# Kernel optimization log

Measured on AMD Instinct MI355X. Metric: run time of the kernel, lower is better.

## Reference

```python
import jax, jax.numpy as jnp
import numpy as np

D_MODEL = 1024
N_HEADS = 16
D_HEAD = D_MODEL // N_HEADS
QLEN = 512
MLEN = 512
BATCH = 8


def setup_inputs() -> dict:
    key = jax.random.key(0)
    ks = jax.random.split(key, 12)
    s = 0.02
    inputs = jax.random.normal(ks[0], (QLEN, BATCH, D_MODEL), jnp.float32)
    r = jax.random.normal(ks[1], (QLEN + MLEN, 1, D_MODEL), jnp.float32)
    u = jax.random.normal(ks[2], (N_HEADS, D_HEAD), jnp.float32) * s
    v = jax.random.normal(ks[3], (N_HEADS, D_HEAD), jnp.float32) * s
    mem = jax.random.normal(ks[4], (MLEN, BATCH, D_MODEL), jnp.float32)
    # attention params (Transformer-XL style): fused qkv, r-projection, output proj
    W_qkv = jax.random.normal(ks[5], (D_MODEL, 3 * D_MODEL), jnp.float32) * s
    W_r = jax.random.normal(ks[6], (D_MODEL, D_MODEL), jnp.float32) * s
    W_o = jax.random.normal(ks[7], (D_MODEL, D_MODEL), jnp.float32) * s
    # GRU params: input-hidden and hidden-hidden for gates (r, z, n), torch layout
    W_ih = jax.random.normal(ks[8], (3 * D_MODEL, D_MODEL), jnp.float32) * s
    W_hh = jax.random.normal(ks[9], (3 * D_MODEL, D_MODEL), jnp.float32) * s
    b_ih = jax.random.normal(ks[10], (3 * D_MODEL,), jnp.float32) * s
    b_hh = jax.random.normal(ks[11], (3 * D_MODEL,), jnp.float32) * s
    h0 = jnp.zeros((BATCH, D_MODEL), jnp.float32)
    return dict(inputs=inputs, r=r, u=u, v=v, mem=mem, W_qkv=W_qkv, W_r=W_r,
                W_o=W_o, W_ih=W_ih, W_hh=W_hh, b_ih=b_ih, b_hh=b_hh, h0=h0)


def _rel_shift(x):
    # x: [q, k, b, h] -> Transformer-XL relative shift
    q, k, b, h = x.shape
    zero_pad = jnp.zeros((q, 1, b, h), x.dtype)
    x_padded = jnp.concatenate([zero_pad, x], axis=1)        # [q, k+1, b, h]
    x_padded = x_padded.reshape(k + 1, q, b, h)
    return x_padded[1:].reshape(q, k, b, h)


def _attention(inputs, r, u, v, mem, W_qkv, W_r, W_o):
    qlen, bsz, _ = inputs.shape
    cat = jnp.concatenate([mem, inputs], axis=0)             # [klen, b, d]
    klen = cat.shape[0]
    qkv = cat @ W_qkv                                        # [klen, b, 3d]
    w_head_q, w_head_k, w_head_v = jnp.split(qkv, 3, axis=-1)
    w_head_q = w_head_q[-qlen:]                              # [q, b, d]
    r_head_k = (r[:, 0, :] @ W_r).reshape(klen, N_HEADS, D_HEAD)  # [k, h, dh]

    q_ = w_head_q.reshape(qlen, bsz, N_HEADS, D_HEAD)
    k_ = w_head_k.reshape(klen, bsz, N_HEADS, D_HEAD)
    v_ = w_head_v.reshape(klen, bsz, N_HEADS, D_HEAD)

    AC = jnp.einsum('ibhd,jbhd->ijbh', q_ + u[None, None], k_)
    BD = jnp.einsum('ibhd,jhd->ijbh', q_ + v[None, None], r_head_k)
    BD = _rel_shift(BD)
    scale = 1.0 / np.sqrt(D_HEAD)
    attn_score = (AC + BD) * scale                           # [q, k, b, h]

    # causal mask with memory: query i attends to keys j <= i + mlen
    mlen = klen - qlen
    i = jnp.arange(qlen)[:, None]
    j = jnp.arange(klen)[None, :]
    mask = j > (i + mlen)                                    # [q, k]
    attn_score = jnp.where(mask[:, :, None, None], -jnp.inf, attn_score)

    attn_prob = jax.nn.softmax(attn_score, axis=1)
    attn_vec = jnp.einsum('ijbh,jbhd->ibhd', attn_prob, v_)
    attn_vec = attn_vec.reshape(qlen, bsz, D_MODEL)
    return attn_vec @ W_o                                    # [q, b, d]


def _gru(x, h0, W_ih, W_hh, b_ih, b_hh):
    # x: [T, B, D]; torch GRU cell math
    Wi_r, Wi_z, Wi_n = jnp.split(W_ih, 3, axis=0)
    Wh_r, Wh_z, Wh_n = jnp.split(W_hh, 3, axis=0)
    bi_r, bi_z, bi_n = jnp.split(b_ih, 3)
    bh_r, bh_z, bh_n = jnp.split(b_hh, 3)

    # precompute input projections for all timesteps
    xr = x @ Wi_r.T + bi_r
    xz = x @ Wi_z.T + bi_z
    xn = x @ Wi_n.T + bi_n

    def step(h, xs):
        xr_t, xz_t, xn_t = xs
        r = jax.nn.sigmoid(xr_t + h @ Wh_r.T + bh_r)
        z = jax.nn.sigmoid(xz_t + h @ Wh_z.T + bh_z)
        n = jnp.tanh(xn_t + r * (h @ Wh_n.T + bh_n))
        h_new = (1.0 - z) * n + z * h
        return h_new, h_new

    _, ys = jax.lax.scan(step, h0, (xr, xz, xn))
    return ys                                                # [T, B, D]


def reference(inputs, r, u, v, mem, W_qkv, W_r, W_o, W_ih, W_hh, b_ih, b_hh, h0):
    y = _attention(inputs, r, u, v, mem, W_qkv, W_r, W_o)
    return _gru(y, h0, W_ih, W_hh, b_ih, b_hh)
```

## Files before the change

### kernel.cpp

```cpp
#include <hip/hip_runtime.h>
#include <math.h>


typedef short bf16x8 __attribute__((ext_vector_type(8)));
typedef float f32x4 __attribute__((ext_vector_type(4)));

union FragU { uint4 u; bf16x8 h; };

__device__ inline void split2(float x0, float x1, unsigned& hi, unsigned& lo) {
    unsigned u0 = __float_as_uint(x0), u1 = __float_as_uint(x1);
    float h0 = __uint_as_float(u0 & 0xffff0000u);
    float h1 = __uint_as_float(u1 & 0xffff0000u);
    unsigned l0 = __float_as_uint(x0 - h0), l1 = __float_as_uint(x1 - h1);
    hi = (u0 >> 16) | (u1 & 0xffff0000u);
    lo = (l0 >> 16) | (l1 & 0xffff0000u);
}

template<bool TR>
__global__ __launch_bounds__(256) void prep_w(
    const float* __restrict__ W, unsigned* __restrict__ out, int Nr, int K, int ldw)
{
    int idx = blockIdx.x * 256 + threadIdx.x;
    int cpr = K >> 3;
    if (idx >= Nr * cpr) return;
    int n, c;
    if (TR) { n = idx % Nr; c = idx / Nr; }
    else    { c = idx % cpr; n = idx / cpr; }
    int kt = c >> 2, j = c & 3;
    int k = kt * 32 + j * 8;
    float x[8];
    #pragma unroll
    for (int i = 0; i < 8; ++i)
        x[i] = TR ? W[(size_t)(k + i) * ldw + n] : W[(size_t)n * ldw + k + i];
    unsigned h[4], l[4];
    split2(x[0], x[1], h[0], l[0]);
    split2(x[2], x[3], h[1], l[1]);
    split2(x[4], x[5], h[2], l[2]);
    split2(x[6], x[7], h[3], l[3]);
    unsigned* base = out + (size_t)n * K + kt * 32;
    *(uint4*)(base + (((2 * j) ^ (n & 7)) * 4))     = make_uint4(h[0], h[1], h[2], h[3]);
    *(uint4*)(base + (((2 * j + 1) ^ (n & 7)) * 4)) = make_uint4(l[0], l[1], l[2], l[3]);
}

template<int AMODE, bool BIAS>
__global__ __launch_bounds__(256) void gemm_mfma(
    const float* __restrict__ A, const float* __restrict__ A2,
    const unsigned* __restrict__ Bp, const float* __restrict__ bias,
    float* __restrict__ C, int M, int N, int K, int lda, int ldc)
{
    __shared__ uint4 Ab[1024];
    __shared__ uint4 Bb[1024];
    int tid = threadIdx.x;
    int lane = tid & 63, wid = tid >> 6;
    int wr = wid >> 1, wc = wid & 1;
    int n0 = blockIdx.x * 128, m0 = blockIdx.y * 128;
    int r15 = lane & 15, s = lane >> 4;

    f32x4 acc[4][4];
    #pragma unroll
    for (int i = 0; i < 4; ++i)
        #pragma unroll
        for (int j = 0; j < 4; ++j) acc[i][j] = 0.0f;

    for (int kt = 0; kt < (K >> 5); ++kt) {
        int k0 = kt * 32;
        #pragma unroll
        for (int q = 0; q < 2; ++q) {
            int idx = q * 256 + tid;
            int row = idx >> 2, j = idx & 3;
            const float* ap;
            if (AMODE == 1) {
                int gm = m0 + row;
                ap = (gm < 4096) ? (A + (size_t)gm * lda) : (A2 + (size_t)(gm - 4096) * lda);
            } else {
                ap = A + (size_t)(m0 + row) * lda;
            }
            float4 x0 = *(const float4*)(ap + k0 + j * 8);
            float4 x1 = *(const float4*)(ap + k0 + j * 8 + 4);
            unsigned h[4], l[4];
            split2(x0.x, x0.y, h[0], l[0]);
            split2(x0.z, x0.w, h[1], l[1]);
            split2(x1.x, x1.y, h[2], l[2]);
            split2(x1.z, x1.w, h[3], l[3]);
            Ab[row * 8 + (((2 * j) ^ (row & 7)))]     = make_uint4(h[0], h[1], h[2], h[3]);
            Ab[row * 8 + (((2 * j + 1) ^ (row & 7)))] = make_uint4(l[0], l[1], l[2], l[3]);
        }
        #pragma unroll
        for (int q = 0; q < 4; ++q) {
            int idx = q * 256 + tid;
            int row = idx >> 3, slot = idx & 7;
            Bb[idx] = *(const uint4*)(Bp + (size_t)(n0 + row) * K + k0 + slot * 4);
        }
        __syncthreads();
        FragU ahi[4], alo[4], bhi[4], blo[4];
        #pragma unroll
        for (int f = 0; f < 4; ++f) {
            int ar = wr * 64 + f * 16 + r15;
            ahi[f].u = Ab[ar * 8 + ((2 * s) ^ (ar & 7))];
            alo[f].u = Ab[ar * 8 + ((2 * s + 1) ^ (ar & 7))];
            int br = wc * 64 + f * 16 + r15;
            bhi[f].u = Bb[br * 8 + ((2 * s) ^ (br & 7))];
            blo[f].u = Bb[br * 8 + ((2 * s + 1) ^ (br & 7))];
        }
        #pragma unroll
        for (int fi = 0; fi < 4; ++fi)
            #pragma unroll
            for (int fj = 0; fj < 4; ++fj) {
                acc[fi][fj] = __builtin_amdgcn_mfma_f32_16x16x32_bf16(ahi[fi].h, bhi[fj].h, acc[fi][fj], 0, 0, 0);
                acc[fi][fj] = __builtin_amdgcn_mfma_f32_16x16x32_bf16(ahi[fi].h, blo[fj].h, acc[fi][fj], 0, 0, 0);
                acc[fi][fj] = __builtin_amdgcn_mfma_f32_16x16x32_bf16(alo[fi].h, bhi[fj].h, acc[fi][fj], 0, 0, 0);
            }
        __syncthreads();
    }
    int r4 = (lane >> 4) * 4;
    #pragma unroll
    for (int fj = 0; fj < 4; ++fj) {
        int n = n0 + wc * 64 + fj * 16 + r15;
        float bv = BIAS ? bias[n] : 0.f;
        #pragma unroll
        for (int fi = 0; fi < 4; ++fi) {
            int m = m0 + wr * 64 + fi * 16 + r4;
            #pragma unroll
            for (int r = 0; r < 4; ++r)
                C[(size_t)(m + r) * ldc + n] = acc[fi][fj][r] + bv;
        }
    }
}

__global__ __launch_bounds__(256) void attn_fused(
    const float* __restrict__ qkv, const float* __restrict__ rk,
    const float* __restrict__ u_, const float* __restrict__ v_,
    float* __restrict__ y1)
{
    __shared__ float qu[64][68], qv[64][68], Kt[64][68], Vt[64][68];
    __shared__ float RKs[128][68];
    __shared__ float S[64][68];
    __shared__ float mrow[64], lrow[64], scalef[64];
    __shared__ float pmax[64][16], psum[64][16];

    int tid = threadIdx.x;
    int it = blockIdx.x, b = blockIdx.y, h = blockIdx.z;
    int i0 = it * 64;
    int ti = tid >> 4, tj = tid & 15;

    {
        int r = tid >> 2, c0 = (tid & 3) * 16;
        size_t base = ((size_t)(i0 + r + 512) * 8 + b) * 3072 + h * 64;
        #pragma unroll
        for (int q = 0; q < 4; ++q) {
            int c = c0 + q * 4;
            float4 qq = *(const float4*)&qkv[base + c];
            float4 uu = *(const float4*)&u_[h * 64 + c];
            float4 vv = *(const float4*)&v_[h * 64 + c];
            *(float4*)&qu[r][c] = make_float4(qq.x + uu.x, qq.y + uu.y, qq.z + uu.z, qq.w + uu.w);
            *(float4*)&qv[r][c] = make_float4(qq.x + vv.x, qq.y + vv.y, qq.z + vv.z, qq.w + vv.w);
        }
    }
    if (tid < 64) { mrow[tid] = -1e30f; lrow[tid] = 0.f; }

    float Od[4][4] = {};
    int njt = it + 9;

    for (int jt = 0; jt < njt; ++jt) {
        int j0 = jt * 64;
        __syncthreads();
        {
            int r = tid >> 2, c0 = (tid & 3) * 16;
            size_t kb = ((size_t)(j0 + r) * 8 + b) * 3072 + 1024 + h * 64;
            #pragma unroll
            for (int q = 0; q < 4; ++q) {
                int c = c0 + q * 4;
                *(float4*)&Kt[r][c] = *(const float4*)&qkv[kb + c];
                *(float4*)&Vt[r][c] = *(const float4*)&qkv[kb + 1024 + c];
            }
        }
        {
            int r2 = tid >> 1, c0 = (tid & 1) * 32;
            int jj = j0 - i0 + 448 + r2;
            jj = jj < 0 ? 0 : (jj > 1023 ? 1023 : jj);
            size_t rb = (size_t)jj * 1024 + h * 64;
            #pragma unroll
            for (int q = 0; q < 8; ++q) {
                int c = c0 + q * 4;
                *(float4*)&RKs[r2][c] = *(const float4*)&rk[rb + c];
            }
        }
        __syncthreads();

        float acc[4][4] = {};
        int jlb = (tj - ti) * 4 + 60;
        #pragma unroll 4
        for (int d4 = 0; d4 < 64; d4 += 4) {
            float4 Aq[4], Cq[4], Kv[4], Rv[7];
            #pragma unroll
            for (int i = 0; i < 4; ++i) {
                Aq[i] = *(float4*)&qu[ti * 4 + i][d4];
                Cq[i] = *(float4*)&qv[ti * 4 + i][d4];
                Kv[i] = *(float4*)&Kt[tj * 4 + i][d4];
            }
            #pragma unroll
            for (int t = 0; t < 7; ++t)
                Rv[t] = *(float4*)&RKs[jlb + t][d4];
            #pragma unroll
            for (int i = 0; i < 4; ++i)
                #pragma unroll
                for (int j = 0; j < 4; ++j) {
                    float4 kk = Kv[j];
                    float4 rr = Rv[j - i + 3];
                    acc[i][j] += Aq[i].x * kk.x + Aq[i].y * kk.y + Aq[i].z * kk.z + Aq[i].w * kk.w
                               + Cq[i].x * rr.x + Cq[i].y * rr.y + Cq[i].z * rr.z + Cq[i].w * rr.w;
                }
        }
        #pragma unroll
        for (int i = 0; i < 4; ++i) {
            int gi = i0 + ti * 4 + i;
            float mx = -1e30f;
            #pragma unroll
            for (int j = 0; j < 4; ++j) {
                int gj = j0 + tj * 4 + j;
                float vS = acc[i][j] * 0.125f;
                if (gj > gi + 512) vS = -1e30f;
                acc[i][j] = vS;
                mx = fmaxf(mx, vS);
            }
            pmax[ti * 4 + i][tj] = mx;
        }
        __syncthreads();
        if (tid < 64) {
            float mo = mrow[tid], mn = mo;
            #pragma unroll
            for (int t = 0; t < 16; ++t) mn = fmaxf(mn, pmax[tid][t]);
            mrow[tid] = mn;
            scalef[tid] = __expf(mo - mn);
        }
        __syncthreads();
        #pragma unroll
        for (int i = 0; i < 4; ++i) {
            int ri = ti * 4 + i;
            float mn = mrow[ri];
            float4 pv;
            pv.x = __expf(acc[i][0] - mn);
            pv.y = __expf(acc[i][1] - mn);
            pv.z = __expf(acc[i][2] - mn);
            pv.w = __expf(acc[i][3] - mn);
            *(float4*)&S[ri][tj * 4] = pv;
            psum[ri][tj] = pv.x + pv.y + pv.z + pv.w;
            float scl = scalef[ri];
            #pragma unroll
            for (int j2 = 0; j2 < 4; ++j2) Od[i][j2] *= scl;
        }
        __syncthreads();
        if (tid < 64) {
            float s = 0.f;
            #pragma unroll
            for (int t = 0; t < 16; ++t) s += psum[tid][t];
            lrow[tid] = lrow[tid] * scalef[tid] + s;
        }
        #pragma unroll 4
        for (int jb = 0; jb < 64; jb += 4) {
            float4 p0 = *(float4*)&S[ti * 4 + 0][jb];
            float4 p1 = *(float4*)&S[ti * 4 + 1][jb];
            float4 p2 = *(float4*)&S[ti * 4 + 2][jb];
            float4 p3 = *(float4*)&S[ti * 4 + 3][jb];
            float4 v0 = *(float4*)&Vt[jb + 0][tj * 4];
            float4 v1 = *(float4*)&Vt[jb + 1][tj * 4];
            float4 v2 = *(float4*)&Vt[jb + 2][tj * 4];
            float4 v3 = *(float4*)&Vt[jb + 3][tj * 4];
            float4 pr[4] = {p0, p1, p2, p3};
            #pragma unroll
            for (int i = 0; i < 4; ++i) {
                Od[i][0] += pr[i].x * v0.x + pr[i].y * v1.x + pr[i].z * v2.x + pr[i].w * v3.x;
                Od[i][1] += pr[i].x * v0.y + pr[i].y * v1.y + pr[i].z * v2.y + pr[i].w * v3.y;
                Od[i][2] += pr[i].x * v0.z + pr[i].y * v1.z + pr[i].z * v2.z + pr[i].w * v3.z;
                Od[i][3] += pr[i].x * v0.w + pr[i].y * v1.w + pr[i].z * v2.w + pr[i].w * v3.w;
            }
        }
    }
    __syncthreads();
    #pragma unroll
    for (int i = 0; i < 4; ++i) {
        int ri = ti * 4 + i;
        float inv = 1.f / lrow[ri];
        float4 o = make_float4(Od[i][0] * inv, Od[i][1] * inv, Od[i][2] * inv, Od[i][3] * inv);
        *(float4*)&y1[((size_t)(i0 + ri) * 8 + b) * 1024 + h * 64 + tj * 4] = o;
    }
}

__global__ __launch_bounds__(256) void prep_whh(
    const float* __restrict__ Whh, uint4* __restrict__ outp)
{
    int idx = blockIdx.x * 256 + threadIdx.x;
    if (idx >= 393216) return;
    int lane = idx & 63;
    int rest = idx >> 6;
    int gate = rest % 3;
    int kt   = (rest / 3) & 31;
    int g64  = rest / 96;
    int n = gate * 1024 + g64 * 16 + (lane & 15);
    int k = kt * 32 + (lane >> 4) * 8;
    const float* src = Whh + (size_t)n * 1024 + k;
    float4 x0 = *(const float4*)src, x1 = *(const float4*)(src + 4);
    unsigned h[4], l[4];
    split2(x0.x, x0.y, h[0], l[0]);
    split2(x0.z, x0.w, h[1], l[1]);
    split2(x1.x, x1.y, h[2], l[2]);
    split2(x1.z, x1.w, h[3], l[3]);
    outp[((size_t)rest * 2 + 0) * 64 + lane] = make_uint4(h[0], h[1], h[2], h[3]);
    outp[((size_t)rest * 2 + 1) * 64 + lane] = make_uint4(l[0], l[1], l[2], l[3]);
}

__global__ __launch_bounds__(192, 1) void gru_step_mfma(
    const float* __restrict__ hin, float* __restrict__ hout,
    const uint4* __restrict__ WhhG, const float* __restrict__ bhh,
    const float* __restrict__ xg, float* __restrict__ out, int t)
{
    __shared__ uint4 Bf[4096];
    __shared__ float red[3][64][4];
    int tid = threadIdx.x;
    int lane = tid & 63, wv = tid >> 6;
    int g64 = blockIdx.x;

    int col = lane & 15;
    int d0 = g64 * 16 + (lane >> 4) * 4;
    bool act = (wv == 0) && (col < 8);
    float4 xr4, xz4, xn4, hp4, br4, bz4, bn4;
    if (act) {
        size_t xb = ((size_t)t * 8 + col) * 3072 + d0;
        xr4 = *(const float4*)&xg[xb];
        xz4 = *(const float4*)&xg[xb + 1024];
        xn4 = *(const float4*)&xg[xb + 2048];
        hp4 = *(const float4*)&hin[col * 1024 + d0];
        br4 = *(const float4*)&bhh[d0];
        bz4 = *(const float4*)&bhh[1024 + d0];
        bn4 = *(const float4*)&bhh[2048 + d0];
    }

    const uint4* wb = WhhG + (size_t)g64 * 12288 + wv * 128 + lane;

    uint4 wA[16], wB[16];
    #pragma unroll
    for (int q = 0; q < 8; ++q) {
        wA[2 * q]     = wb[(0 * 8 + q) * 384];
        wA[2 * q + 1] = wb[(0 * 8 + q) * 384 + 64];
    }

    for (int s = tid; s < 1024; s += 192) {
        int b = s & 7, oct = (s >> 3) & 3, kt = s >> 5;
        const float* hp = hin + b * 1024 + kt * 32 + oct * 8;
        float4 x0 = *(const float4*)hp, x1 = *(const float4*)(hp + 4);
        unsigned hh[4], ll[4];
        split2(x0.x, x0.y, hh[0], ll[0]);
        split2(x0.z, x0.w, hh[1], ll[1]);
        split2(x1.x, x1.y, hh[2], ll[2]);
        split2(x1.z, x1.w, hh[3], ll[3]);
        int ln = oct * 16 + b;
        Bf[(kt * 2 + 0) * 64 + ln] = make_uint4(hh[0], hh[1], hh[2], hh[3]);
        Bf[(kt * 2 + 1) * 64 + ln] = make_uint4(ll[0], ll[1], ll[2], ll[3]);
    }
    __syncthreads();

    f32x4 acc = 0.0f;
    #define GRU_LOAD(dst, c0)                                   \
        _Pragma("unroll")                                       \
        for (int q = 0; q < 8; ++q) {                           \
            dst[2 * q]     = wb[((c0) * 8 + q) * 384];          \
            dst[2 * q + 1] = wb[((c0) * 8 + q) * 384 + 64];     \
        }
    #define GRU_COMP(src, c0)                                   \
        _Pragma("unroll")                                       \
        for (int q = 0; q < 8; ++q) {                           \
            int kt = (c0) * 8 + q;                              \
            FragU ah, al, bh, bl;                               \
            ah.u = src[2 * q]; al.u = src[2 * q + 1];           \
            bh.u = Bf[(kt * 2 + 0) * 64 + lane];                \
            bl.u = Bf[(kt * 2 + 1) * 64 + lane];                \
            acc = __builtin_amdgcn_mfma_f32_16x16x32_bf16(ah.h, bh.h, acc, 0, 0, 0); \
            acc = __builtin_amdgcn_mfma_f32_16x16x32_bf16(ah.h, bl.h, acc, 0, 0, 0); \
            acc = __builtin_amdgcn_mfma_f32_16x16x32_bf16(al.h, bh.h, acc, 0, 0, 0); \
        }
    GRU_LOAD(wB, 1);
    GRU_COMP(wA, 0);
    GRU_LOAD(wA, 2);
    GRU_COMP(wB, 1);
    GRU_LOAD(wB, 3);
    GRU_COMP(wA, 2);
    GRU_COMP(wB, 3);
    #undef GRU_LOAD
    #undef GRU_COMP

    *(f32x4*)&red[wv][lane][0] = acc;
    __syncthreads();

    if (act) {
        f32x4 aR = *(f32x4*)&red[0][lane][0];
        f32x4 aZ = *(f32x4*)&red[1][lane][0];
        f32x4 aN = *(f32x4*)&red[2][lane][0];
        float xr[4] = {xr4.x, xr4.y, xr4.z, xr4.w};
        float xz[4] = {xz4.x, xz4.y, xz4.z, xz4.w};
        float xn[4] = {xn4.x, xn4.y, xn4.z, xn4.w};
        float hp[4] = {hp4.x, hp4.y, hp4.z, hp4.w};
        float br[4] = {br4.x, br4.y, br4.z, br4.w};
        float bz[4] = {bz4.x, bz4.y, bz4.z, bz4.w};
        float bn[4] = {bn4.x, bn4.y, bn4.z, bn4.w};
        float hn[4];
        #pragma unroll
        for (int r = 0; r < 4; ++r) {
            float rr = 1.f / (1.f + __expf(-(xr[r] + aR[r] + br[r])));
            float zz = 1.f / (1.f + __expf(-(xz[r] + aZ[r] + bz[r])));
            float nn = tanhf(xn[r] + rr * (aN[r] + bn[r]));
            hn[r] = (1.f - zz) * nn + zz * hp[r];
        }
        float4 hv = make_float4(hn[0], hn[1], hn[2], hn[3]);
        *(float4*)&hout[col * 1024 + d0] = hv;
        *(float4*)&out[((size_t)t * 8 + col) * 1024 + d0] = hv;
    }
}

extern "C" void kernel_launch(void* const* d_in, const int* in_sizes, int n_in,
                              void* d_out, int out_size, void* d_ws, size_t ws_size,
                              hipStream_t stream) {
    (void)in_sizes; (void)n_in; (void)out_size; (void)ws_size;
    const float* inputs = (const float*)d_in[0];
    const float* r_in   = (const float*)d_in[1];
    const float* u_in   = (const float*)d_in[2];
    const float* v_in   = (const float*)d_in[3];
    const float* mem    = (const float*)d_in[4];
    const float* Wqkv   = (const float*)d_in[5];
    const float* Wr     = (const float*)d_in[6];
    const float* Wo     = (const float*)d_in[7];
    const float* Wih    = (const float*)d_in[8];
    const float* Whh    = (const float*)d_in[9];
    const float* bih    = (const float*)d_in[10];
    const float* bhh    = (const float*)d_in[11];
    const float* h0     = (const float*)d_in[12];
    float* out = (float*)d_out;
    float* ws = (float*)d_ws;

    float*    qkv   = ws;
    float*    rk    = ws + 25165824;
    float*    y1    = ws + 26214400;
    float*    y2    = ws + 30408704;
    float*    xg    = ws + 34603008;
    float*    hA    = ws + 47185920;
    float*    hB    = ws + 47194112;
    unsigned* WqkvP = (unsigned*)(ws + 47202304);
    unsigned* WrP   = (unsigned*)(ws + 50348032);
    unsigned* WoP   = (unsigned*)(ws + 51396608);
    unsigned* WihP  = (unsigned*)(ws + 52445184);
    uint4*    WhhG  = (uint4*)qkv;

    dim3 blk(256);
    prep_w<true ><<<1536, blk, 0, stream>>>(Wqkv, WqkvP, 3072, 1024, 3072);
    prep_w<true ><<< 512, blk, 0, stream>>>(Wr,   WrP,   1024, 1024, 1024);
    prep_w<true ><<< 512, blk, 0, stream>>>(Wo,   WoP,   1024, 1024, 1024);
    prep_w<false><<<1536, blk, 0, stream>>>(Wih,  WihP,  3072, 1024, 1024);

    gemm_mfma<1, false><<<dim3(24, 64), blk, 0, stream>>>(
        mem, inputs, WqkvP, nullptr, qkv, 8192, 3072, 1024, 1024, 3072);
    gemm_mfma<0, false><<<dim3(8, 8), blk, 0, stream>>>(
        r_in, nullptr, WrP, nullptr, rk, 1024, 1024, 1024, 1024, 1024);
    attn_fused<<<dim3(8, 8, 16), blk, 0, stream>>>(qkv, rk, u_in, v_in, y1);
    prep_whh<<<1536, blk, 0, stream>>>(Whh, WhhG);
    gemm_mfma<0, false><<<dim3(8, 32), blk, 0, stream>>>(
        y1, nullptr, WoP, nullptr, y2, 4096, 1024, 1024, 1024, 1024);
    gemm_mfma<0, true><<<dim3(24, 32), blk, 0, stream>>>(
        y2, nullptr, WihP, bih, xg, 4096, 3072, 1024, 1024, 3072);

    const float* hin = h0;
    for (int s = 0; s < 512; ++s) {
        float* hp = (s & 1) ? hB : hA;
        gru_step_mfma<<<64, dim3(192), 0, stream>>>(hin, hp, WhhG, bhh, xg, out, s);
        hin = hp;
    }
}
```

Baseline: 5.219 ms.

## Replace per-step GRU kernel launches with a persistent cooperative kernel

The 512 sequential GRU step launches become one cooperative kernel of 64 blocks. Blocks exchange hidden state through coherent atomic loads and stores and synchronise each step with a flag-based grid barrier. This removes per-launch overhead and kernel boundaries, at the cost of spin-waiting. The per-step launch loop remains as a fallback if the cooperative launch fails.

```diff
diff --git a/kernel.cpp b/kernel.cpp
--- a/kernel.cpp
+++ b/kernel.cpp
@@ -14,6 +14,15 @@
     unsigned l0 = __float_as_uint(x0 - h0), l1 = __float_as_uint(x1 - h1);
     hi = (u0 >> 16) | (u1 & 0xffff0000u);
     lo = (l0 >> 16) | (l1 & 0xffff0000u);
+}
+
+__device__ __forceinline__ unsigned long long ld_coh64(const void* p) {
+    return __hip_atomic_load((const unsigned long long*)p, __ATOMIC_RELAXED,
+                             __HIP_MEMORY_SCOPE_AGENT);
+}
+__device__ __forceinline__ void st_coh64(void* p, unsigned long long v) {
+    __hip_atomic_store((unsigned long long*)p, v, __ATOMIC_RELAXED,
+                       __HIP_MEMORY_SCOPE_AGENT);
 }
 
 template<bool TR>
@@ -309,6 +318,164 @@
     outp[((size_t)rest * 2 + 1) * 64 + lane] = make_uint4(l[0], l[1], l[2], l[3]);
 }
 
+__global__ __launch_bounds__(256, 1) void gru_persist2(
+    const float* __restrict__ h0, float* __restrict__ hA, float* __restrict__ hB,
+    const uint4* __restrict__ WhhG, const float* __restrict__ bhh,
+    const float* __restrict__ xg, float* __restrict__ out,
+    unsigned* __restrict__ flags)
+{
+    __shared__ uint4 Bf[4096];
+    __shared__ float red[3][64][4];
+    int tid = threadIdx.x;
+    int lane = tid & 63, wv = tid >> 6;
+    int g64 = blockIdx.x;
+
+    int col = lane & 15;
+    int d0 = g64 * 16 + (lane >> 4) * 4;
+    bool act = (wv == 0) && (col < 8);
+    float4 br4 = make_float4(0, 0, 0, 0), bz4 = br4, bn4 = br4;
+    if (act) {
+        br4 = *(const float4*)&bhh[d0];
+        bz4 = *(const float4*)&bhh[1024 + d0];
+        bn4 = *(const float4*)&bhh[2048 + d0];
+    }
+    const uint4* wb = WhhG + (size_t)g64 * 12288 + (wv < 3 ? wv : 0) * 128 + lane;
+
+    for (int t = 0; t < 512; ++t) {
+        const float* hi_ = (t == 0) ? h0 : ((t & 1) ? hA : hB);
+        float* ho = (t & 1) ? hB : hA;
+
+        float4 xr4, xz4, xn4;
+        unsigned long long hp01 = 0, hp23 = 0;
+        if (act) {
+            size_t xb = ((size_t)t * 8 + col) * 3072 + d0;
+            xr4 = *(const float4*)&xg[xb];
+            xz4 = *(const float4*)&xg[xb + 1024];
+            xn4 = *(const float4*)&xg[xb + 2048];
+            hp01 = ld_coh64(hi_ + col * 1024 + d0);
+            hp23 = ld_coh64(hi_ + col * 1024 + d0 + 2);
+        }
+
+        uint4 wA[16], wB[16];
+        #pragma unroll
+        for (int q = 0; q < 8; ++q) {
+            wA[2 * q]     = wb[q * 384];
+            wA[2 * q + 1] = wb[q * 384 + 64];
+        }
+
+        unsigned long long hq[16];
+        #pragma unroll
+        for (int i = 0; i < 4; ++i) {
+            int s = i * 256 + tid;
+            const float* hp = hi_ + (s & 7) * 1024 + (s >> 5) * 32 + ((s >> 3) & 3) * 8;
+            #pragma unroll
+            for (int q = 0; q < 4; ++q) hq[i * 4 + q] = ld_coh64(hp + q * 2);
+        }
+        #pragma unroll
+        for (int i = 0; i < 4; ++i) {
+            int s = i * 256 + tid;
+            int b = s & 7, oct = (s >> 3) & 3, kt = s >> 5;
+            float x[8];
+            #pragma unroll
+            for (int q = 0; q < 4; ++q) {
+                x[2 * q]     = __uint_as_float((unsigned)(hq[i * 4 + q] & 0xffffffffu));
+                x[2 * q + 1] = __uint_as_float((unsigned)(hq[i * 4 + q] >> 32));
+            }
+            unsigned hh[4], ll[4];
+            split2(x[0], x[1], hh[0], ll[0]);
+            split2(x[2], x[3], hh[1], ll[1]);
+            split2(x[4], x[5], hh[2], ll[2]);
+            split2(x[6], x[7], hh[3], ll[3]);
+            int ln = oct * 16 + b;
+            Bf[(kt * 2 + 0) * 64 + ln] = make_uint4(hh[0], hh[1], hh[2], hh[3]);
+            Bf[(kt * 2 + 1) * 64 + ln] = make_uint4(ll[0], ll[1], ll[2], ll[3]);
+        }
+        __syncthreads();
+
+        f32x4 acc = 0.0f;
+        #define GRU_LOAD(dst, c0)                                   \
+            _Pragma("unroll")                                       \
+            for (int q = 0; q < 8; ++q) {                           \
+                dst[2 * q]     = wb[((c0) * 8 + q) * 384];          \
+                dst[2 * q + 1] = wb[((c0) * 8 + q) * 384 + 64];     \
+            }
+        #define GRU_COMP(src, c0)                                   \
+            _Pragma("unroll")                                       \
+            for (int q = 0; q < 8; ++q) {                           \
+                int kt = (c0) * 8 + q;                              \
+                FragU ah, al, bh, bl;                               \
+                ah.u = src[2 * q]; al.u = src[2 * q + 1];           \
+                bh.u = Bf[(kt * 2 + 0) * 64 + lane];                \
+                bl.u = Bf[(kt * 2 + 1) * 64 + lane];                \
+                acc = __builtin_amdgcn_mfma_f32_16x16x32_bf16(ah.h, bh.h, acc, 0, 0, 0); \
+                acc = __builtin_amdgcn_mfma_f32_16x16x32_bf16(ah.h, bl.h, acc, 0, 0, 0); \
+                acc = __builtin_amdgcn_mfma_f32_16x16x32_bf16(al.h, bh.h, acc, 0, 0, 0); \
+            }
+        if (wv < 3) {
+            GRU_LOAD(wB, 1);
+            GRU_COMP(wA, 0);
+            GRU_LOAD(wA, 2);
+            GRU_COMP(wB, 1);
+            GRU_LOAD(wB, 3);
+            GRU_COMP(wA, 2);
+            GRU_COMP(wB, 3);
+            *(f32x4*)&red[wv][lane][0] = acc;
+        }
+        #undef GRU_LOAD
+        #undef GRU_COMP
+        __syncthreads();
+
+        if (act) {
+            f32x4 aR = *(f32x4*)&red[0][lane][0];
+            f32x4 aZ = *(f32x4*)&red[1][lane][0];
+            f32x4 aN = *(f32x4*)&red[2][lane][0];
+            float xr[4] = {xr4.x, xr4.y, xr4.z, xr4.w};
+            float xz[4] = {xz4.x, xz4.y, xz4.z, xz4.w};
+            float xn[4] = {xn4.x, xn4.y, xn4.z, xn4.w};
+            float hp[4] = {__uint_as_float((unsigned)(hp01 & 0xffffffffu)),
+                           __uint_as_float((unsigned)(hp01 >> 32)),
+                           __uint_as_float((unsigned)(hp23 & 0xffffffffu)),
+                           __uint_as_float((unsigned)(hp23 >> 32))};
+            float br[4] = {br4.x, br4.y, br4.z, br4.w};
+            float bz[4] = {bz4.x, bz4.y, bz4.z, bz4.w};
+            float bn[4] = {bn4.x, bn4.y, bn4.z, bn4.w};
+            float hn[4];
+            #pragma unroll
+            for (int r = 0; r < 4; ++r) {
+                float rr = 1.f / (1.f + __expf(-(xr[r] + aR[r] + br[r])));
+                float zz = 1.f / (1.f + __expf(-(xz[r] + aZ[r] + bz[r])));
+                float nn = tanhf(xn[r] + rr * (aN[r] + bn[r]));
+                hn[r] = (1.f - zz) * nn + zz * hp[r];
+            }
+            unsigned long long v01 = (unsigned long long)__float_as_uint(hn[0])
+                                   | ((unsigned long long)__float_as_uint(hn[1]) << 32);
+            unsigned long long v23 = (unsigned long long)__float_as_uint(hn[2])
+                                   | ((unsigned long long)__float_as_uint(hn[3]) << 32);
+            st_coh64(ho + col * 1024 + d0, v01);
+            st_coh64(ho + col * 1024 + d0 + 2, v23);
+            *(float4*)&out[((size_t)t * 8 + col) * 1024 + d0] =
+                make_float4(hn[0], hn[1], hn[2], hn[3]);
+        }
+
+        if (t != 511) {
+            __syncthreads();
+            unsigned tgt = (unsigned)t + 1u;
+            if (tid < 64) {
+                if (tid == 0)
+                    __hip_atomic_store(&flags[(size_t)g64 * 16], tgt,
+                                       __ATOMIC_RELAXED, __HIP_MEMORY_SCOPE_AGENT);
+                const unsigned* fp = &flags[(size_t)tid * 16];
+                for (;;) {
+                    unsigned f = __hip_atomic_load(fp, __ATOMIC_RELAXED,
+                                                   __HIP_MEMORY_SCOPE_AGENT);
+                    if (__all(f >= tgt)) break;
+                }
+            }
+            __syncthreads();
+        }
+    }
+}
+
 __global__ __launch_bounds__(192, 1) void gru_step_mfma(
     const float* __restrict__ hin, float* __restrict__ hout,
     const uint4* __restrict__ WhhG, const float* __restrict__ bhh,
@@ -336,12 +503,11 @@
     }
 
     const uint4* wb = WhhG + (size_t)g64 * 12288 + wv * 128 + lane;
-
     uint4 wA[16], wB[16];
     #pragma unroll
     for (int q = 0; q < 8; ++q) {
-        wA[2 * q]     = wb[(0 * 8 + q) * 384];
-        wA[2 * q + 1] = wb[(0 * 8 + q) * 384 + 64];
+        wA[2 * q]     = wb[q * 384];
+        wA[2 * q + 1] = wb[q * 384 + 64];
     }
 
     for (int s = tid; s < 1024; s += 192) {
@@ -447,6 +613,7 @@
     unsigned* WrP   = (unsigned*)(ws + 50348032);
     unsigned* WoP   = (unsigned*)(ws + 51396608);
     unsigned* WihP  = (unsigned*)(ws + 52445184);
+    unsigned* flags = (unsigned*)(ws + 55590912);
     uint4*    WhhG  = (uint4*)qkv;
 
     dim3 blk(256);
@@ -454,6 +621,7 @@
     prep_w<true ><<< 512, blk, 0, stream>>>(Wr,   WrP,   1024, 1024, 1024);
     prep_w<true ><<< 512, blk, 0, stream>>>(Wo,   WoP,   1024, 1024, 1024);
     prep_w<false><<<1536, blk, 0, stream>>>(Wih,  WihP,  3072, 1024, 1024);
+    hipMemsetAsync(flags, 0, 4096, stream);
 
     gemm_mfma<1, false><<<dim3(24, 64), blk, 0, stream>>>(
         mem, inputs, WqkvP, nullptr, qkv, 8192, 3072, 1024, 1024, 3072);
@@ -466,10 +634,20 @@
     gemm_mfma<0, true><<<dim3(24, 32), blk, 0, stream>>>(
         y2, nullptr, WihP, bih, xg, 4096, 3072, 1024, 1024, 3072);
 
-    const float* hin = h0;
-    for (int s = 0; s < 512; ++s) {
-        float* hp = (s & 1) ? hB : hA;
-        gru_step_mfma<<<64, dim3(192), 0, stream>>>(hin, hp, WhhG, bhh, xg, out, s);
-        hin = hp;
-    }
-}
+    {
+        const float* a0 = h0; float* a1 = hA; float* a2 = hB;
+        const uint4* a3 = WhhG; const float* a4 = bhh; const float* a5 = xg;
+        float* a6 = out; unsigned* a7 = flags;
+        void* args[8] = {&a0, &a1, &a2, &a3, &a4, &a5, &a6, &a7};
+        hipError_t e = hipLaunchCooperativeKernel((void*)gru_persist2,
+                                                  dim3(64), dim3(256), args, 0, stream);
+        if (e != hipSuccess) {
+            const float* hin = h0;
+            for (int s = 0; s < 512; ++s) {
+                float* hp = (s & 1) ? hB : hA;
+                gru_step_mfma<<<64, dim3(192), 0, stream>>>(hin, hp, WhhG, bhh, xg, out, s);
+                hin = hp;
+            }
+        }
+    }
+}
```

After: 4.737 ms. 1.1x faster.
